# Kernel tuning notes

Measured on AMD Instinct MI355X. Metric: run time of the kernel, lower is better.

The kernel has to match this reference:

```python
import jax, jax.numpy as jnp
import numpy as np

N, F, H, ATTR = 128, 128, 8, 3
HU, HUE = [16, 8], [4, 2]


def setup_inputs() -> dict:
    key = jax.random.key(0)
    ks = iter(jax.random.split(key, 40))
    def g(shape):
        return jax.random.normal(next(ks), shape, dtype=jnp.float32) * 0.1
    M = N * N
    return dict(
        X=g((N, F)), A=g((ATTR, N, N)), E=g((ATTR, N, N)), e2n_adj=g((N, M)),
        Wn0=g((ATTR, H, F, HU[0])), bn0=jnp.zeros((ATTR, H, HU[0]), jnp.float32),
        an0_s=g((ATTR, H, HU[0])), an0_n=g((ATTR, H, HU[0])),
        Wn1=g((ATTR, H, H * HU[0], HU[1])), bn1=jnp.zeros((ATTR, H, HU[1]), jnp.float32),
        an1_s=g((ATTR, H, HU[1])), an1_n=g((ATTR, H, HU[1])),
        We0=g((H, ATTR, HUE[0])), be0=jnp.zeros((H, HUE[0]), jnp.float32),
        We1=g((H, H * HUE[0], HUE[1])), be1=jnp.zeros((H, HUE[1]), jnp.float32),
        Wct0=g((H, HU[0] + HUE[0], HU[0])), bct0=jnp.zeros((H, HU[0]), jnp.float32),
        Wct1=g((H, HU[1] + HUE[1], HU[1])), bct1=jnp.zeros((H, HU[1]), jnp.float32),
        ae0_s=g((H, HU[0])), ae0_n=g((H, HUE[0])),
        ae1_s=g((H, HU[1])), ae1_n=g((H, HUE[1])),
    )


def _leaky(x):
    return jnp.where(x >= 0, x, 0.2 * x)  # LeakyReLU(0.2)


def reference(X, A, E, e2n_adj,
              Wn0, bn0, an0_s, an0_n, Wn1, bn1, an1_s, an1_n,
              We0, be0, We1, be1, Wct0, bct0, Wct1, bct1,
              ae0_s, ae0_n, ae1_s, ae1_n):
    # Eval mode (dropout = identity). Heads are vectorized (leading h axis).
    nb_attr, n = E.shape[0], X.shape[0]
    E_e2n = E.reshape(nb_attr, -1).T  # [M, nb_attr], row-major flatten matches torch .view(-1,1)
    edge_layers = [(We0, be0, Wct0, bct0, ae0_s, ae0_n),
                   (We1, be1, Wct1, bct1, ae1_s, ae1_n)]
    attrs_out = []
    for attr in range(nb_attr):
        node_layers = [(Wn0[attr], bn0[attr], an0_s[attr], an0_n[attr]),
                       (Wn1[attr], bn1[attr], an1_s[attr], an1_n[attr])]
        X_head, X_edge, E_info = X, E_e2n, E[attr]
        h_list = [X]
        for (Wn, bn, an_s, an_n), (We, be, Wct, bct, ae_s, ae_n) in zip(node_layers, edge_layers):
            feat = jnp.einsum('nf,hfk->hnk', X_head, Wn)          # node features per head
            feat_e = jnp.einsum('mf,hfk->hmk', X_edge, We)        # edge features per head
            a_self = jnp.einsum('hnk,hk->hn', feat, ae_s)
            a_edge = jnp.einsum('hmk,hk->hm', feat_e, ae_n)
            # edge-to-node attention over all M = N*N edges
            alpha_e = jax.nn.softmax(_leaky(a_self[:, :, None] + a_edge[:, None, :]) + e2n_adj[None], axis=-1)
            nf_e = jnp.einsum('hnm,hmk->hnk', alpha_e, feat_e) + be[:, None, :]
            feat2 = jnp.einsum('hnc,hck->hnk', jnp.concatenate([feat, nf_e], axis=-1), Wct) + bct[:, None, :]
            s2 = jnp.einsum('hnk,hk->hn', feat2, an_s)
            n2 = jnp.einsum('hnk,hk->hn', feat2, an_n)
            dense = jnp.einsum('hij,jm->him', s2[:, :, None] + n2[:, None, :], E_info)  # [h,N,N]
            alpha = jax.nn.softmax(_leaky(dense) + A[attr][None], axis=-1)
            nf = jax.nn.elu(jnp.einsum('hnm,hmk->hnk', alpha, feat2) + bn[:, None, :])
            h1 = jnp.transpose(nf, (1, 0, 2)).reshape(n, -1)      # concat heads on feature axis
            h_list.append(h1)
            X_head = h1
            X_edge = jnp.transpose(feat_e, (1, 0, 2)).reshape(feat_e.shape[1], -1)
            E_info = alpha[-1]                                    # last head's attention matrix
        attrs_out.append(jnp.concatenate(h_list, axis=-1)[:, None, :])
    return jnp.concatenate(attrs_out, axis=1)                     # [N, nb_attr, F + 8*16 + 8*8]
```

## Files before the change

### kernel.cpp

```cpp
#include <hip/hip_runtime.h>

static constexpr int N = 128;
static constexpr int F = 128;
static constexpr int H = 8;
static constexpr int NATTR = 3;
static constexpr int M = N * N;
static constexpr int OUTW = 320;
static constexpr int MSL = 32;
static constexpr int CH = M / MSL;
static constexpr float LOG2E = 1.4426950408889634f;

__device__ __forceinline__ float leaky(float x) { return fmaxf(x, 0.2f * x); }

template <int KE, bool L1>
__global__ void __launch_bounds__(256)
k_ea(const float* __restrict__ E,
     const float* __restrict__ xsrc,
     int xStride,
     const float* __restrict__ Wn,
     const float* __restrict__ aes,
     const float* __restrict__ We0,
     const float* __restrict__ aen,
     const float* __restrict__ We1,
     const float* __restrict__ adj,
     float* __restrict__ part) {
    constexpr int KW = L1 ? 8 : 16;
    __shared__ __align__(16) float sFe[4 * CH * KE];
    __shared__ __align__(16) float sAe[4 * CH];
    __shared__ __align__(16) float sWv[12 * 128];
    __shared__ __align__(16) float sWc[48];

    int b = blockIdx.x;
    int ms = b & (MSL - 1);
    int nt = (b >> 5) & 7;
    int h0 = (b >> 8) * 4;
    int tid = threadIdx.x;
    int r = tid >> 4, l = tid & 15;
    int n = nt * 16 + r;
    int m0 = ms * CH;

    for (int idx = tid; idx < 12 * 128; idx += 256) {
        int c = idx >> 7, f = idx & 127;
        int a = c >> 2, h = h0 + (c & 3);
        const float* wp = Wn + ((size_t)(a * H + h) * F + f) * KW;
        const float* ap = aes + h * KW;
        float acc = 0.f;
#pragma unroll
        for (int k = 0; k < KW; ++k) acc += wp[k] * ap[k];
        sWv[idx] = acc * LOG2E;
    }
    if (L1) {
        if (tid < 24) {
            int hh = tid / 6, rem = tid % 6, at = rem >> 1, k2 = rem & 1;
            int h = h0 + hh;
            float acc = 0.f;
            for (int c = 0; c < 32; ++c)
                acc += We0[((c >> 2) * 3 + at) * 4 + (c & 3)] *
                       We1[(h * 32 + c) * 2 + k2];
            sWc[(hh * 3 + at) * 2 + k2] = acc;
        }
        __syncthreads();
    }
    for (int idx = tid; idx < 4 * CH; idx += 256) {
        int hh = idx >> 9, mm = idx & (CH - 1);
        int m = m0 + mm, h = h0 + hh;
        float e0 = E[m], e1 = E[M + m], e2 = E[2 * M + m];
        if (!L1) {
            float aa = 0.f;
#pragma unroll
            for (int k = 0; k < 4; ++k) {
                float f = e0 * We0[(h * 3 + 0) * 4 + k] +
                          e1 * We0[(h * 3 + 1) * 4 + k] +
                          e2 * We0[(h * 3 + 2) * 4 + k];
                sFe[(hh * CH + mm) * 4 + k] = f;
                aa += f * aen[h * 4 + k];
            }
            sAe[hh * CH + mm] = aa * LOG2E;
        } else {
            float f0 = e0 * sWc[(hh * 3 + 0) * 2 + 0] + e1 * sWc[(hh * 3 + 1) * 2 + 0] +
                       e2 * sWc[(hh * 3 + 2) * 2 + 0];
            float f1 = e0 * sWc[(hh * 3 + 0) * 2 + 1] + e1 * sWc[(hh * 3 + 1) * 2 + 1] +
                       e2 * sWc[(hh * 3 + 2) * 2 + 1];
            sFe[(hh * CH + mm) * 2 + 0] = f0;
            sFe[(hh * CH + mm) * 2 + 1] = f1;
            sAe[hh * CH + mm] = (f0 * aen[h * 2 + 0] + f1 * aen[h * 2 + 1]) * LOG2E;
        }
    }
    __syncthreads();

    float as[NATTR][4];
#pragma unroll
    for (int a = 0; a < NATTR; ++a) {
        const float* xr = xsrc + (size_t)a * xStride + (size_t)n * F;
        float xv[8];
#pragma unroll
        for (int j = 0; j < 8; ++j) xv[j] = xr[l + 16 * j];
#pragma unroll
        for (int hh = 0; hh < 4; ++hh) {
            const float* wr = sWv + (a * 4 + hh) * 128;
            float d = 0.f;
#pragma unroll
            for (int j = 0; j < 8; ++j) d += xv[j] * wr[l + 16 * j];
#pragma unroll
            for (int off = 1; off < 16; off <<= 1) d += __shfl_xor(d, off);
            as[a][hh] = d;
        }
    }

    float sum[4][NATTR];
    float acc[4][NATTR][KE];
#pragma unroll
    for (int hh = 0; hh < 4; ++hh)
#pragma unroll
        for (int a = 0; a < NATTR; ++a) {
            sum[hh][a] = 0.f;
#pragma unroll
            for (int k = 0; k < KE; ++k) acc[hh][a][k] = 0.f;
        }

    const float* adjp = adj + (size_t)n * M + m0;
    for (int i = l * 4; i < CH; i += 64) {
        const float4 av = *(const float4*)(adjp + i);
        float4 ev[4];
#pragma unroll
        for (int hh = 0; hh < 4; ++hh)
            ev[hh] = *(const float4*)&sAe[hh * CH + i];
#pragma unroll
        for (int j = 0; j < 4; ++j) {
            float adjv = (&av.x)[j] * LOG2E;
#pragma unroll
            for (int hh = 0; hh < 4; ++hh) {
                float aev = (&ev[hh].x)[j];
                float fv[KE];
                if (KE == 4) {
                    const float4 fq = *(const float4*)&sFe[(hh * CH + i + j) * 4];
                    fv[0] = fq.x; fv[1] = fq.y; fv[2] = fq.z; fv[3] = fq.w;
                } else {
                    const float2 fq = *(const float2*)&sFe[(hh * CH + i + j) * 2];
                    fv[0] = fq.x; fv[1] = fq.y;
                }
#pragma unroll
                for (int a = 0; a < NATTR; ++a) {
                    float t = as[a][hh] + aev;
                    float p = __builtin_amdgcn_exp2f(fmaxf(t, 0.2f * t) + adjv);
                    sum[hh][a] += p;
#pragma unroll
                    for (int k = 0; k < KE; ++k) acc[hh][a][k] += p * fv[k];
                }
            }
        }
    }

#pragma unroll
    for (int off = 1; off < 16; off <<= 1) {
#pragma unroll
        for (int hh = 0; hh < 4; ++hh)
#pragma unroll
            for (int a = 0; a < NATTR; ++a) {
                sum[hh][a] += __shfl_xor(sum[hh][a], off);
#pragma unroll
                for (int k = 0; k < KE; ++k) acc[hh][a][k] += __shfl_xor(acc[hh][a][k], off);
            }
    }
    if (l == 0) {
#pragma unroll
        for (int hh = 0; hh < 4; ++hh)
#pragma unroll
            for (int a = 0; a < NATTR; ++a) {
                float* pp = part + (((size_t)(a * H + h0 + hh) * N + n) * MSL + ms) * 8;
#pragma unroll
                for (int k = 0; k < KE; ++k) pp[k] = acc[hh][a][k];
                pp[7] = sum[hh][a];
            }
    }
}

template <int K, int KE, bool FIRST>
__global__ void __launch_bounds__(256)
k_mid(const float* __restrict__ xsrc,
      int xStride,
      const float* __restrict__ Wn,
      const float* __restrict__ part,
      const float* __restrict__ be,
      const float* __restrict__ Wct,
      const float* __restrict__ bct,
      const float* __restrict__ ans,
      const float* __restrict__ ann,
      const float* __restrict__ X,
      float* __restrict__ out,
      float* __restrict__ feat2,
      float* __restrict__ s2,
      float* __restrict__ n2) {
    constexpr int CIN = K + KE;
    __shared__ __align__(16) float sWn[F * K];
    __shared__ __align__(16) float sW[CIN * K];
    __shared__ __align__(16) float sIn[32 * CIN];
    __shared__ __align__(16) float sF2[32 * K];

    int b = blockIdx.x;
    int nt = b & 3, h = (b >> 2) & 7, a = b >> 5;
    int n0 = nt * 32;
    int tid = threadIdx.x;

    for (int i = tid; i < F * K; i += 256)
        sWn[i] = Wn[(size_t)(a * H + h) * F * K + i];
    for (int i = tid; i < CIN * K; i += 256) sW[i] = Wct[h * CIN * K + i];

    {
        int r = tid >> 3, g = tid & 7;
        int n = n0 + r;
        const float* pp = part + ((size_t)(a * H + h) * N + n) * MSL * 8;
        float av[4] = {0.f, 0.f, 0.f, 0.f};
        float sv = 0.f;
        for (int ms = g; ms < MSL; ms += 8) {
            const float4 x = *(const float4*)(pp + ms * 8);
            const float4 y = *(const float4*)(pp + ms * 8 + 4);
            av[0] += x.x; av[1] += x.y;
            if (KE == 4) { av[2] += x.z; av[3] += x.w; }
            sv += y.w;
        }
#pragma unroll
        for (int off = 1; off < 8; off <<= 1) {
#pragma unroll
            for (int k = 0; k < KE; ++k) av[k] += __shfl_xor(av[k], off);
            sv += __shfl_xor(sv, off);
        }
        if (g == 0) {
            float inv = 1.f / sv;
#pragma unroll
            for (int k = 0; k < KE; ++k)
                sIn[r * CIN + K + k] = av[k] * inv + be[h * KE + k];
        }
    }
    if (FIRST && h == 0) {
        for (int i = tid; i < 32 * F; i += 256) {
            int n = n0 + (i >> 7);
            int f = i & (F - 1);
            out[(n * NATTR + a) * OUTW + f] = X[n * F + f];
        }
    }
    __syncthreads();

    for (int o = tid; o < 32 * K; o += 256) {
        int r = o / K, k = o % K;
        const float* xr = xsrc + (size_t)a * xStride + (size_t)(n0 + r) * F;
        float acc = 0.f;
        for (int f = 0; f < F; ++f) acc += xr[f] * sWn[f * K + k];
        sIn[r * CIN + k] = acc;
    }
    __syncthreads();

    for (int o = tid; o < 32 * K; o += 256) {
        int r = o / K, k = o % K;
        float acc = bct[h * K + k];
        for (int c = 0; c < CIN; ++c) acc += sIn[r * CIN + c] * sW[c * K + k];
        sF2[o] = acc;
        feat2[((size_t)(a * H + h) * N + n0 + r) * 16 + k] = acc;
    }
    __syncthreads();
    if (tid < 32) {
        int r = tid;
        float ss = 0.f, nn = 0.f;
        for (int k = 0; k < K; ++k) {
            ss += sF2[r * K + k] * ans[(a * H + h) * K + k];
            nn += sF2[r * K + k] * ann[(a * H + h) * K + k];
        }
        s2[(a * H + h) * N + n0 + r] = ss;
        n2[(a * H + h) * N + n0 + r] = nn;
    }
}

template <int K, bool FIRST>
__global__ void __launch_bounds__(256)
k_node(const float* __restrict__ feat2,
       const float* __restrict__ s2,
       const float* __restrict__ n2,
       const float* __restrict__ Einfo,
       const float* __restrict__ Amat,
       const float* __restrict__ bn,
       float* __restrict__ out, int outOff,
       float* __restrict__ xh_out,
       float* __restrict__ einfo_out) {
    __shared__ __align__(16) float sF2[N * K];
    __shared__ __align__(16) float sS2[N];
    __shared__ __align__(16) float sn2[N];
    __shared__ __align__(16) float sdE[N];
    __shared__ __align__(16) float scE[N];
    __shared__ __align__(16) float sAlpha[4 * N];
    __shared__ __align__(16) float sRed[256];

    int b = blockIdx.x;
    int itile = b & 7, h = (b >> 3) & 7, a = b >> 6;
    int tid = threadIdx.x;

    for (int i = tid; i < N * K; i += 256)
        sF2[i] = feat2[((size_t)(a * H + h) * N + i / K) * 16 + i % K];
    if (tid < N) {
        sS2[tid] = s2[(a * H + h) * N + tid];
        sn2[tid] = n2[(a * H + h) * N + tid];
    }
    __syncthreads();

    {
        int m = tid & 127, w = tid >> 7;
        const float* Ep = Einfo + (size_t)a * M;
        float dacc = 0.f, cacc = 0.f;
        for (int j = w * 64; j < w * 64 + 64; ++j) {
            float v = Ep[j * N + m];
            dacc += sn2[j] * v;
            cacc += v;
        }
        sRed[tid] = dacc;
        sAlpha[w * N + m] = cacc;
        __syncthreads();
        if (tid < N) {
            sdE[tid] = sRed[tid] + sRed[128 + tid];
            scE[tid] = sAlpha[tid] + sAlpha[N + tid];
        }
    }
    __syncthreads();

    for (int pass = 0; pass < 4; ++pass) {
        int r = tid >> 6;
        int lane = tid & 63;
        int i = itile * 16 + pass * 4 + r;
        float s = sS2[i];
        const float* Ap = Amat + ((size_t)a * N + i) * N;
        float v0 = leaky(s * scE[lane] + sdE[lane]) + Ap[lane];
        float v1 = leaky(s * scE[lane + 64] + sdE[lane + 64]) + Ap[lane + 64];
        float p0 = __expf(v0), p1 = __expf(v1);
        float ssum = p0 + p1;
#pragma unroll
        for (int off = 1; off < 64; off <<= 1) ssum += __shfl_xor(ssum, off);
        float inv = 1.f / ssum;
        float a0 = p0 * inv, a1 = p1 * inv;
        sAlpha[r * N + lane] = a0;
        sAlpha[r * N + lane + 64] = a1;
        if (FIRST && h == H - 1) {
            einfo_out[((size_t)a * N + i) * N + lane] = a0;
            einfo_out[((size_t)a * N + i) * N + lane + 64] = a1;
        }
        __syncthreads();
        {
            int rr = tid >> 6, g = (tid >> 4) & 3, k = tid & 15;
            float acc = 0.f;
            if (k < K) {
                for (int it = 0; it < 32; ++it) {
                    int mm = g + 4 * it;
                    acc += sAlpha[rr * N + mm] * sF2[mm * K + k];
                }
            }
            sRed[tid] = acc;
        }
        __syncthreads();
        {
            int rr = tid >> 6, k = tid & 63;
            if (k < K) {
                float tot = bn[(a * H + h) * K + k];
#pragma unroll
                for (int g = 0; g < 4; ++g) tot += sRed[rr * 64 + g * 16 + k];
                float e = tot > 0.f ? tot : __expf(tot) - 1.f;
                int i2 = itile * 16 + pass * 4 + rr;
                out[(i2 * NATTR + a) * OUTW + outOff + h * K + k] = e;
                if (FIRST)
                    xh_out[((size_t)a * N + i2) * F + h * K + k] = e;
            }
        }
        __syncthreads();
    }
}

extern "C" void kernel_launch(void* const* d_in, const int* in_sizes, int n_in,
                              void* d_out, int out_size, void* d_ws, size_t ws_size,
                              hipStream_t stream) {
    const float* X    = (const float*)d_in[0];
    const float* A    = (const float*)d_in[1];
    const float* E    = (const float*)d_in[2];
    const float* adj  = (const float*)d_in[3];
    const float* Wn0  = (const float*)d_in[4];
    const float* bn0  = (const float*)d_in[5];
    const float* an0s = (const float*)d_in[6];
    const float* an0n = (const float*)d_in[7];
    const float* Wn1  = (const float*)d_in[8];
    const float* bn1  = (const float*)d_in[9];
    const float* an1s = (const float*)d_in[10];
    const float* an1n = (const float*)d_in[11];
    const float* We0  = (const float*)d_in[12];
    const float* be0  = (const float*)d_in[13];
    const float* We1  = (const float*)d_in[14];
    const float* be1  = (const float*)d_in[15];
    const float* Wct0 = (const float*)d_in[16];
    const float* bct0 = (const float*)d_in[17];
    const float* Wct1 = (const float*)d_in[18];
    const float* bct1 = (const float*)d_in[19];
    const float* ae0s = (const float*)d_in[20];
    const float* ae0n = (const float*)d_in[21];
    const float* ae1s = (const float*)d_in[22];
    const float* ae1n = (const float*)d_in[23];
    float* out = (float*)d_out;

    float* p = (float*)d_ws;
    float* part  = p; p += (size_t)NATTR * H * N * MSL * 8;
    float* feat2 = p; p += NATTR * H * N * 16;
    float* s2b   = p; p += NATTR * H * N;
    float* n2b   = p; p += NATTR * H * N;
    float* einfo = p; p += NATTR * N * N;
    float* xh    = p; p += NATTR * N * F;

    k_ea<4, false><<<dim3(512), dim3(256), 0, stream>>>(
        E, X, 0, Wn0, ae0s, We0, ae0n, nullptr, adj, part);
    k_mid<16, 4, true><<<dim3(96), dim3(256), 0, stream>>>(
        X, 0, Wn0, part, be0, Wct0, bct0, an0s, an0n, X, out,
        feat2, s2b, n2b);
    k_node<16, true><<<dim3(192), dim3(256), 0, stream>>>(
        feat2, s2b, n2b, E, A, bn0, out, F, xh, einfo);

    k_ea<2, true><<<dim3(512), dim3(256), 0, stream>>>(
        E, xh, N * F, Wn1, ae1s, We0, ae1n, We1, adj, part);
    k_mid<8, 2, false><<<dim3(96), dim3(256), 0, stream>>>(
        xh, N * F, Wn1, part, be1, Wct1, bct1, an1s, an1n, nullptr, nullptr,
        feat2, s2b, n2b);
    k_node<8, false><<<dim3(192), dim3(256), 0, stream>>>(
        feat2, s2b, n2b, einfo, A, bn1, out, F + 128, nullptr, nullptr);
}
```

Measured before the change: 86.29 us.

## Accumulate raw edge-attribute moments and apply edge weights after softmax reduction

Edge features are linear in the three edge attributes, so the edge-attention kernel now accumulates softmax-weighted sums of the raw attributes (3 moments plus the normaliser) instead of per-head projected features. The We0/We1 projection moves into the mid kernel and runs once per row. This shrinks shared memory per block (one shared attribute array instead of per-head feature arrays), which is used to double the M slicing to 64 and launch twice as many blocks. The partials layout becomes a single float4 per head, written with one vector store, and an XOR swizzle is added on the shared attribute array to reduce bank conflicts. The price is more partials for the mid kernel to reduce and a small recomputation of the combined edge weights there.

```diff
diff --git a/kernel.cpp b/kernel.cpp
--- a/kernel.cpp
+++ b/kernel.cpp
@@ -6,13 +6,14 @@
 static constexpr int NATTR = 3;
 static constexpr int M = N * N;
 static constexpr int OUTW = 320;
-static constexpr int MSL = 32;
+static constexpr int MSL = 64;
 static constexpr int CH = M / MSL;
 static constexpr float LOG2E = 1.4426950408889634f;
 
 __device__ __forceinline__ float leaky(float x) { return fmaxf(x, 0.2f * x); }
-
-template <int KE, bool L1>
+__device__ __forceinline__ int swz(int m) { return m ^ ((m >> 3) & 7); }
+
+template <bool L1>
 __global__ void __launch_bounds__(256)
 k_ea(const float* __restrict__ E,
      const float* __restrict__ xsrc,
@@ -25,15 +26,16 @@
      const float* __restrict__ adj,
      float* __restrict__ part) {
     constexpr int KW = L1 ? 8 : 16;
-    __shared__ __align__(16) float sFe[4 * CH * KE];
-    __shared__ __align__(16) float sAe[4 * CH];
+    __shared__ __align__(16) float sV[4 * CH];
+    __shared__ __align__(16) float sEx[CH * 4];
     __shared__ __align__(16) float sWv[12 * 128];
-    __shared__ __align__(16) float sWc[48];
+    __shared__ float sVa[12];
+    __shared__ float sWc[24];
 
     int b = blockIdx.x;
     int ms = b & (MSL - 1);
-    int nt = (b >> 5) & 7;
-    int h0 = (b >> 8) * 4;
+    int nt = (b >> 6) & 7;
+    int h0 = (b >> 9) * 4;
     int tid = threadIdx.x;
     int r = tid >> 4, l = tid & 15;
     int n = nt * 16 + r;
@@ -61,34 +63,41 @@
         }
         __syncthreads();
     }
-    for (int idx = tid; idx < 4 * CH; idx += 256) {
-        int hh = idx >> 9, mm = idx & (CH - 1);
-        int m = m0 + mm, h = h0 + hh;
+    if (tid < 12) {
+        int hh = tid >> 2 == 0 ? tid / 3 : tid / 3;
+        int at = tid % 3;
+        hh = tid / 3;
+        int h = h0 + hh;
+        float acc = 0.f;
+        if (!L1) {
+#pragma unroll
+            for (int k = 0; k < 4; ++k)
+                acc += We0[(h * 3 + at) * 4 + k] * aen[h * 4 + k];
+        } else {
+#pragma unroll
+            for (int k2 = 0; k2 < 2; ++k2)
+                acc += sWc[(hh * 3 + at) * 2 + k2] * aen[h * 2 + k2];
+        }
+        sVa[hh * 3 + at] = acc * LOG2E;
+    }
+    __syncthreads();
+
+    for (int mm = tid; mm < CH; mm += 256) {
+        int m = m0 + mm;
         float e0 = E[m], e1 = E[M + m], e2 = E[2 * M + m];
-        if (!L1) {
-            float aa = 0.f;
-#pragma unroll
-            for (int k = 0; k < 4; ++k) {
-                float f = e0 * We0[(h * 3 + 0) * 4 + k] +
-                          e1 * We0[(h * 3 + 1) * 4 + k] +
-                          e2 * We0[(h * 3 + 2) * 4 + k];
-                sFe[(hh * CH + mm) * 4 + k] = f;
-                aa += f * aen[h * 4 + k];
-            }
-            sAe[hh * CH + mm] = aa * LOG2E;
-        } else {
-            float f0 = e0 * sWc[(hh * 3 + 0) * 2 + 0] + e1 * sWc[(hh * 3 + 1) * 2 + 0] +
-                       e2 * sWc[(hh * 3 + 2) * 2 + 0];
-            float f1 = e0 * sWc[(hh * 3 + 0) * 2 + 1] + e1 * sWc[(hh * 3 + 1) * 2 + 1] +
-                       e2 * sWc[(hh * 3 + 2) * 2 + 1];
-            sFe[(hh * CH + mm) * 2 + 0] = f0;
-            sFe[(hh * CH + mm) * 2 + 1] = f1;
-            sAe[hh * CH + mm] = (f0 * aen[h * 2 + 0] + f1 * aen[h * 2 + 1]) * LOG2E;
-        }
-    }
-    __syncthreads();
-
-    float as[NATTR][4];
+        int mw = swz(mm);
+        sEx[mw * 4 + 0] = e0;
+        sEx[mw * 4 + 1] = e1;
+        sEx[mw * 4 + 2] = e2;
+        sEx[mw * 4 + 3] = 0.f;
+#pragma unroll
+        for (int hh = 0; hh < 4; ++hh)
+            sV[hh * CH + mm] = sVa[hh * 3 + 0] * e0 + sVa[hh * 3 + 1] * e1 +
+                               sVa[hh * 3 + 2] * e2;
+    }
+    __syncthreads();
+
+    float u[NATTR][4];
 #pragma unroll
     for (int a = 0; a < NATTR; ++a) {
         const float* xr = xsrc + (size_t)a * xStride + (size_t)n * F;
@@ -103,19 +112,17 @@
             for (int j = 0; j < 8; ++j) d += xv[j] * wr[l + 16 * j];
 #pragma unroll
             for (int off = 1; off < 16; off <<= 1) d += __shfl_xor(d, off);
-            as[a][hh] = d;
-        }
-    }
-
-    float sum[4][NATTR];
-    float acc[4][NATTR][KE];
+            u[a][hh] = d;
+        }
+    }
+
+    float sm[4][NATTR], q0[4][NATTR], q1[4][NATTR], q2[4][NATTR];
 #pragma unroll
     for (int hh = 0; hh < 4; ++hh)
 #pragma unroll
         for (int a = 0; a < NATTR; ++a) {
-            sum[hh][a] = 0.f;
-#pragma unroll
-            for (int k = 0; k < KE; ++k) acc[hh][a][k] = 0.f;
+            sm[hh][a] = 0.f;
+            q0[hh][a] = 0.f; q1[hh][a] = 0.f; q2[hh][a] = 0.f;
         }
 
     const float* adjp = adj + (size_t)n * M + m0;
@@ -124,29 +131,23 @@
         float4 ev[4];
 #pragma unroll
         for (int hh = 0; hh < 4; ++hh)
-            ev[hh] = *(const float4*)&sAe[hh * CH + i];
+            ev[hh] = *(const float4*)&sV[hh * CH + i];
 #pragma unroll
         for (int j = 0; j < 4; ++j) {
             float adjv = (&av.x)[j] * LOG2E;
+            const float4 ex = *(const float4*)&sEx[swz(i + j) * 4];
 #pragma unroll
             for (int hh = 0; hh < 4; ++hh) {
-                float aev = (&ev[hh].x)[j];
-                float fv[KE];
-                if (KE == 4) {
-                    const float4 fq = *(const float4*)&sFe[(hh * CH + i + j) * 4];
-                    fv[0] = fq.x; fv[1] = fq.y; fv[2] = fq.z; fv[3] = fq.w;
-                } else {
-                    const float2 fq = *(const float2*)&sFe[(hh * CH + i + j) * 2];
-                    fv[0] = fq.x; fv[1] = fq.y;
+                float vv = (&ev[hh].x)[j];
+#pragma unroll
+                for (int a = 0; a < NATTR; ++a) {
+                    float t = u[a][hh] + vv;
+                    float p = __builtin_amdgcn_exp2f(fmaxf(t, 0.2f * t) + adjv);
+                    sm[hh][a] += p;
+                    q0[hh][a] += p * ex.x;
+                    q1[hh][a] += p * ex.y;
+                    q2[hh][a] += p * ex.z;
                 }
-#pragma unroll
-                for (int a = 0; a < NATTR; ++a) {
-                    float t = as[a][hh] + aev;
-                    float p = __builtin_amdgcn_exp2f(fmaxf(t, 0.2f * t) + adjv);
-                    sum[hh][a] += p;
-#pragma unroll
-                    for (int k = 0; k < KE; ++k) acc[hh][a][k] += p * fv[k];
-                }
             }
         }
     }
@@ -157,9 +158,10 @@
         for (int hh = 0; hh < 4; ++hh)
 #pragma unroll
             for (int a = 0; a < NATTR; ++a) {
-                sum[hh][a] += __shfl_xor(sum[hh][a], off);
-#pragma unroll
-                for (int k = 0; k < KE; ++k) acc[hh][a][k] += __shfl_xor(acc[hh][a][k], off);
+                sm[hh][a] += __shfl_xor(sm[hh][a], off);
+                q0[hh][a] += __shfl_xor(q0[hh][a], off);
+                q1[hh][a] += __shfl_xor(q1[hh][a], off);
+                q2[hh][a] += __shfl_xor(q2[hh][a], off);
             }
     }
     if (l == 0) {
@@ -167,10 +169,10 @@
         for (int hh = 0; hh < 4; ++hh)
 #pragma unroll
             for (int a = 0; a < NATTR; ++a) {
-                float* pp = part + (((size_t)(a * H + h0 + hh) * N + n) * MSL + ms) * 8;
-#pragma unroll
-                for (int k = 0; k < KE; ++k) pp[k] = acc[hh][a][k];
-                pp[7] = sum[hh][a];
+                float* pp = part + (((size_t)ms * NATTR + a) * N + n) * 32 +
+                            (h0 + hh) * 4;
+                *(float4*)pp = make_float4(q0[hh][a], q1[hh][a], q2[hh][a],
+                                           sm[hh][a]);
             }
     }
 }
@@ -181,6 +183,8 @@
       int xStride,
       const float* __restrict__ Wn,
       const float* __restrict__ part,
+      const float* __restrict__ We0,
+      const float* __restrict__ We1,
       const float* __restrict__ be,
       const float* __restrict__ Wct,
       const float* __restrict__ bct,
@@ -209,27 +213,50 @@
     {
         int r = tid >> 3, g = tid & 7;
         int n = n0 + r;
-        const float* pp = part + ((size_t)(a * H + h) * N + n) * MSL * 8;
-        float av[4] = {0.f, 0.f, 0.f, 0.f};
-        float sv = 0.f;
+        float m0 = 0.f, m1 = 0.f, m2 = 0.f, sv = 0.f;
         for (int ms = g; ms < MSL; ms += 8) {
-            const float4 x = *(const float4*)(pp + ms * 8);
-            const float4 y = *(const float4*)(pp + ms * 8 + 4);
-            av[0] += x.x; av[1] += x.y;
-            if (KE == 4) { av[2] += x.z; av[3] += x.w; }
-            sv += y.w;
+            const float4 v = *(const float4*)(
+                part + (((size_t)ms * NATTR + a) * N + n) * 32 + h * 4);
+            m0 += v.x; m1 += v.y; m2 += v.z; sv += v.w;
         }
 #pragma unroll
         for (int off = 1; off < 8; off <<= 1) {
-#pragma unroll
-            for (int k = 0; k < KE; ++k) av[k] += __shfl_xor(av[k], off);
+            m0 += __shfl_xor(m0, off);
+            m1 += __shfl_xor(m1, off);
+            m2 += __shfl_xor(m2, off);
             sv += __shfl_xor(sv, off);
         }
         if (g == 0) {
             float inv = 1.f / sv;
-#pragma unroll
-            for (int k = 0; k < KE; ++k)
-                sIn[r * CIN + K + k] = av[k] * inv + be[h * KE + k];
+            float mom[3] = {m0, m1, m2};
+            if (KE == 4) {
+#pragma unroll
+                for (int k = 0; k < 4; ++k) {
+                    float acc = 0.f;
+#pragma unroll
+                    for (int at = 0; at < 3; ++at)
+                        acc += We0[(h * 3 + at) * 4 + k] * mom[at];
+                    sIn[r * CIN + K + k] = acc * inv + be[h * 4 + k];
+                }
+            } else {
+                float wc[3][2];
+#pragma unroll
+                for (int at = 0; at < 3; ++at) {
+                    float w0 = 0.f, w1 = 0.f;
+                    for (int c = 0; c < 32; ++c) {
+                        float we0 = We0[((c >> 2) * 3 + at) * 4 + (c & 3)];
+                        w0 += we0 * We1[(h * 32 + c) * 2 + 0];
+                        w1 += we0 * We1[(h * 32 + c) * 2 + 1];
+                    }
+                    wc[at][0] = w0; wc[at][1] = w1;
+                }
+#pragma unroll
+                for (int k = 0; k < 2; ++k) {
+                    float acc = wc[0][k] * mom[0] + wc[1][k] * mom[1] +
+                                wc[2][k] * mom[2];
+                    sIn[r * CIN + K + k] = acc * inv + be[h * 2 + k];
+                }
+            }
         }
     }
     if (FIRST && h == 0) {
@@ -400,26 +427,26 @@
     float* out = (float*)d_out;
 
     float* p = (float*)d_ws;
-    float* part  = p; p += (size_t)NATTR * H * N * MSL * 8;
+    float* part  = p; p += (size_t)MSL * NATTR * N * 32;
     float* feat2 = p; p += NATTR * H * N * 16;
     float* s2b   = p; p += NATTR * H * N;
     float* n2b   = p; p += NATTR * H * N;
     float* einfo = p; p += NATTR * N * N;
     float* xh    = p; p += NATTR * N * F;
 
-    k_ea<4, false><<<dim3(512), dim3(256), 0, stream>>>(
+    k_ea<false><<<dim3(2 * 8 * MSL), dim3(256), 0, stream>>>(
         E, X, 0, Wn0, ae0s, We0, ae0n, nullptr, adj, part);
     k_mid<16, 4, true><<<dim3(96), dim3(256), 0, stream>>>(
-        X, 0, Wn0, part, be0, Wct0, bct0, an0s, an0n, X, out,
+        X, 0, Wn0, part, We0, nullptr, be0, Wct0, bct0, an0s, an0n, X, out,
         feat2, s2b, n2b);
     k_node<16, true><<<dim3(192), dim3(256), 0, stream>>>(
         feat2, s2b, n2b, E, A, bn0, out, F, xh, einfo);
 
-    k_ea<2, true><<<dim3(512), dim3(256), 0, stream>>>(
+    k_ea<true><<<dim3(2 * 8 * MSL), dim3(256), 0, stream>>>(
         E, xh, N * F, Wn1, ae1s, We0, ae1n, We1, adj, part);
     k_mid<8, 2, false><<<dim3(96), dim3(256), 0, stream>>>(
-        xh, N * F, Wn1, part, be1, Wct1, bct1, an1s, an1n, nullptr, nullptr,
-        feat2, s2b, n2b);
+        xh, N * F, Wn1, part, We0, We1, be1, Wct1, bct1, an1s, an1n,
+        nullptr, nullptr, feat2, s2b, n2b);
     k_node<8, false><<<dim3(192), dim3(256), 0, stream>>>(
         feat2, s2b, n2b, einfo, A, bn1, out, F + 128, nullptr, nullptr);
 }
```

Result: slower. 99.69 us (+15.5%).
